# Performance work log

Hardware: AMD Instinct MI355X
Metric: run time of the kernel (lower is better)

## Reference

```python
import jax, jax.numpy as jnp
import numpy as np

B, S, WL = 128, 128, 16
V, C, T = 50000, 100, 17
WE, CE, CF, K, H = 300, 50, 50, 3, 256
D = WE + CF  # LSTM input dim


def setup_inputs() -> dict:
    key = jax.random.key(0)
    ks = jax.random.split(key, 16)
    def n(k, shape, scale=0.05):
        return jax.random.normal(k, shape, jnp.float32) * scale
    words = jax.random.randint(ks[0], (B, S), 0, V)
    chars = jax.random.randint(ks[1], (B, S, WL), 0, C)
    tags = jax.random.randint(ks[2], (B, S), 0, T)
    lengths = jax.random.randint(ks[3], (B,), 1, S + 1)  # at least 1 valid token
    return dict(
        words=words, chars=chars, tags=tags, lengths=lengths,
        word_emb=n(ks[4], (V, WE)).at[0].set(0.0),  # padding_idx=0
        char_emb=n(ks[5], (C, CE)),
        conv_w=n(ks[6], (CF, CE, K)), conv_b=jnp.zeros((CF,), jnp.float32),
        w_ih_f=n(ks[7], (4 * H, D)), w_hh_f=n(ks[8], (4 * H, H)), b_f=jnp.zeros((4 * H,), jnp.float32),
        w_ih_b=n(ks[9], (4 * H, D)), w_hh_b=n(ks[10], (4 * H, H)), b_b=jnp.zeros((4 * H,), jnp.float32),
        proj_w=n(ks[11], (T, 2 * H)), proj_b=jnp.zeros((T,), jnp.float32),
        trans=n(ks[12], (T, T), 0.1), start_trans=n(ks[13], (T,), 0.1), end_trans=n(ks[14], (T,), 0.1),
    )


def _lstm(x, mask, w_ih, w_hh, b):
    # x: [B,S,D], mask: [B,S] bool. PyTorch gate order: i, f, g, o.
    Bh = w_hh.shape[1]
    xg = jnp.einsum('bsd,gd->bsg', x, w_ih) + b  # [B,S,4H]
    def step(carry, inp):
        h, c = carry
        gx, m = inp  # [B,4H], [B]
        g = gx + h @ w_hh.T
        i, f, gg, o = jnp.split(g, 4, axis=-1)
        i = jax.nn.sigmoid(i); f = jax.nn.sigmoid(f)
        gg = jnp.tanh(gg); o = jax.nn.sigmoid(o)
        cn = f * c + i * gg
        hn = o * jnp.tanh(cn)
        m_ = m[:, None]
        return (jnp.where(m_, hn, h), jnp.where(m_, cn, c)), hn * m_
    b_ = x.shape[0]
    init = (jnp.zeros((b_, Bh), x.dtype), jnp.zeros((b_, Bh), x.dtype))
    _, hs = jax.lax.scan(step, init, (jnp.swapaxes(xg, 0, 1), jnp.swapaxes(mask, 0, 1)))
    return jnp.swapaxes(hs, 0, 1)  # [B,S,H]


def _reverse_valid(x, lengths):
    # reverse only the first `length` entries of each row (pack_padded semantics)
    s = x.shape[1]
    t = jnp.arange(s)[None, :]
    idx = jnp.where(t < lengths[:, None], lengths[:, None] - 1 - t, t)
    return jnp.take_along_axis(x, idx[:, :, None], axis=1)


def _crf_nll(emissions, tags, lengths, trans, start_trans, end_trans):
    b, s, t_ = emissions.shape
    mask = jnp.arange(s)[None, :] < lengths[:, None]  # [B,S]
    maskf = mask.astype(emissions.dtype)
    # gold path score
    emit_sc = jnp.take_along_axis(emissions, tags[:, :, None], axis=2)[:, :, 0]  # [B,S]
    score = start_trans[tags[:, 0]] + (emit_sc * maskf).sum(1)
    tr = trans[tags[:, :-1], tags[:, 1:]]  # [B,S-1]
    score = score + (tr * maskf[:, 1:]).sum(1)
    last = jnp.take_along_axis(tags, (lengths - 1)[:, None], axis=1)[:, 0]
    score = score + end_trans[last]
    # partition function (forward algorithm)
    alpha0 = start_trans[None, :] + emissions[:, 0]  # [B,T]
    def step(alpha, inp):
        emit, m = inp  # [B,T], [B]
        nxt = jax.scipy.special.logsumexp(alpha[:, :, None] + trans[None] + emit[:, None, :], axis=1)
        return jnp.where(m[:, None], nxt, alpha), None
    alpha, _ = jax.lax.scan(step, alpha0,
                            (jnp.swapaxes(emissions[:, 1:], 0, 1), jnp.swapaxes(mask[:, 1:], 0, 1)))
    logZ = jax.scipy.special.logsumexp(alpha + end_trans[None, :], axis=-1)
    return jnp.sum(logZ - score)


def reference(words, chars, tags, lengths, word_emb, char_emb, conv_w, conv_b,
              w_ih_f, w_hh_f, b_f, w_ih_b, w_hh_b, b_b, proj_w, proj_b,
              trans, start_trans, end_trans):
    b, s = words.shape
    wl = chars.shape[2]
    we = word_emb[words]  # [B,S,WE]
    ce = char_emb[chars]  # [B,S,WL,CE]
    # CharCNN: conv over word-length, relu, max-pool
    x = ce.reshape(b * s, wl, -1).transpose(0, 2, 1)  # [B*S, CE, WL]
    conv = jax.lax.conv_general_dilated(x, conv_w, (1,), 'SAME',
                                        dimension_numbers=('NCH', 'OIH', 'NCH'))
    conv = conv + conv_b[None, :, None]
    cf = jnp.max(jax.nn.relu(conv), axis=-1).reshape(b, s, -1)  # [B,S,CF]
    inp = jnp.concatenate([we, cf], axis=2)  # [B,S,WE+CF]
    mask = jnp.arange(s)[None, :] < lengths[:, None]
    fwd = _lstm(inp, mask, w_ih_f, w_hh_f, b_f)
    bwd = _reverse_valid(_lstm(_reverse_valid(inp, lengths), mask, w_ih_b, w_hh_b, b_b), lengths)
    h = jnp.concatenate([fwd, bwd], axis=2)  # [B,S,2H]
    emissions = jnp.einsum('bsh,th->bst', h, proj_w) + proj_b
    return _crf_nll(emissions, tags, lengths, trans, start_trans, end_trans)
```

## Files before the change

kernel.cpp:

```cpp
#include <hip/hip_runtime.h>
#include <stdint.h>

typedef unsigned char u8;
typedef unsigned short u16;
typedef unsigned int u32;
typedef unsigned long long u64;

#define NPOS 16384
#define KPAD 384

typedef __attribute__((ext_vector_type(8))) short bf16x8;
typedef __attribute__((ext_vector_type(4))) float f32x4;
typedef __attribute__((ext_vector_type(8))) int i32x8;

__device__ __forceinline__ float bf2f(u16 u) { return __uint_as_float(((u32)u) << 16); }
__device__ __forceinline__ u16 f2bf(float f) {
    u32 u = __float_as_uint(f);
    u += 0x7fffu + ((u >> 16) & 1u);
    return (u16)(u >> 16);
}
__device__ __forceinline__ float frcp(float x) {
#if __has_builtin(__builtin_amdgcn_rcpf)
    return __builtin_amdgcn_rcpf(x);
#else
    return 1.0f / x;
#endif
}
__device__ __forceinline__ float sigm(float x) { return frcp(1.0f + __expf(-x)); }
__device__ __forceinline__ float tanh_(float x) { return fmaf(2.0f, frcp(1.0f + __expf(-2.0f * x)), -1.0f); }

__device__ u8 f2fp8_manual(float f) {
    u32 u = __float_as_uint(f);
    u32 s = (u >> 31) << 7;
    u32 ae = (u >> 23) & 255u;
    u32 m = u & 0x7fffffu;
    int e = (int)ae - 127;
    if (ae == 0) return (u8)s;
    if (e >= 9) return (u8)(s | 0x7e);
    if (e >= -6) {
        u32 mant = m >> 20;
        u32 rem = m & 0xfffffu;
        if (rem > 0x80000u || (rem == 0x80000u && (mant & 1u))) mant++;
        u32 ef = (u32)(e + 7);
        if (mant == 8u) { mant = 0u; ef++; }
        if (ef >= 16u || (ef == 15u && mant == 7u)) return (u8)(s | 0x7e);
        return (u8)(s | (ef << 3) | mant);
    }
    if (e < -10) return (u8)s;
    int sb = 14 - e;
    u32 X = 0x800000u | m;
    u32 mant = X >> sb;
    u32 rem = X & ((1u << sb) - 1u);
    u32 half = 1u << (sb - 1);
    if (rem > half || (rem == half && (mant & 1u))) mant++;
    if (mant >= 8u) return (u8)(s | (1u << 3));
    return (u8)(s | mant);
}

__device__ __forceinline__ u32 f2fp8(float f) {
#if __has_builtin(__builtin_amdgcn_cvt_pk_fp8_f32)
    return (u32)(__builtin_amdgcn_cvt_pk_fp8_f32(f, f, 0, false) & 0xff);
#else
    return (u32)f2fp8_manual(f);
#endif
}

static constexpr size_t OFF_INP  = 0;
static constexpr size_t OFF_WIH  = 12582912;
static constexpr size_t OFF_WHH  = 14155776;
static constexpr size_t OFF_XG   = 15204352;
static constexpr size_t OFF_HS   = 82313216;
static constexpr size_t OFF_EMIS = 99090432;
static constexpr size_t OFF_NLL  = 100204544;
static constexpr size_t OFF_WT   = OFF_XG;

__global__ __launch_bounds__(256) void k_prep0(const float* __restrict__ conv_w,
                                               float* __restrict__ wt) {
    int idx = blockIdx.x * 256 + threadIdx.x;
    if (idx < 7500) {
        int oc = idx / 150, r = idx - oc * 150;
        wt[r * 52 + oc] = conv_w[oc * 150 + r];
    }
}

__global__ __launch_bounds__(256) void k_front(const int* __restrict__ words,
                                               const int* __restrict__ chars,
                                               const float* __restrict__ word_emb,
                                               const float* __restrict__ char_emb,
                                               const float* __restrict__ wt,
                                               const float* __restrict__ conv_b,
                                               u16* __restrict__ inp,
                                               const float* __restrict__ wihf,
                                               const float* __restrict__ wihb,
                                               u16* __restrict__ wih,
                                               const float* __restrict__ whf,
                                               const float* __restrict__ whb,
                                               u8* __restrict__ whh8) {
    __shared__ float ce_t[8][50][20];
    int b = blockIdx.x, tid = threadIdx.x;

    if (b >= 2048) {
        if (b < 3072) {
            int n = (b - 2048) * 2 + (tid >> 7);
            int t128 = tid & 127;
            const float* src = (n < 1024) ? (wihf + (size_t)n * 350) : (wihb + (size_t)(n - 1024) * 350);
            u16* dst = wih + (size_t)n * KPAD;
            for (int k = t128; k < KPAD; k += 128) dst[k] = (k < 350) ? f2bf(src[k]) : (u16)0;
        } else {
            int gr = (b - 3072) * 2 + (tid >> 7);
            int t128 = tid & 127;
            int d = gr >> 10, row = gr & 1023;
            const float* src = (d ? whb : whf) + (size_t)row * 256;
            int g = row >> 8, hid = row & 255;
            int w = hid >> 5, nb = (hid >> 4) & 1, c16 = hid & 15;
            u8* base = whh8 + ((size_t)((d * 8 + w) * 4 + g)) * 8192;
            for (int k = t128; k < 256; k += 128) {
                int kk = k >> 7, q = (k >> 5) & 3, j = k & 31;
                base[((nb * 2 + kk) * 64 + (q * 16 + c16)) * 32 + j] = f2fp8_manual(src[k]);
            }
        }
        return;
    }

    int pos0 = b * 8;

    if (tid < 128) {
        int p = tid >> 4, c = tid & 15;
        int ch = chars[(size_t)(pos0 + p) * 16 + c];
        const float* src = char_emb + (size_t)ch * 50;
#pragma unroll
        for (int i = 0; i < 25; ++i) {
            float2 v = *(const float2*)(src + i * 2);
            ce_t[p][i * 2][c + 1] = v.x;
            ce_t[p][i * 2 + 1][c + 1] = v.y;
        }
    } else {
        int base = tid - 128;
        for (int i = base; i < 1600; i += 128) {
            int p = i / 200, rem = i - p * 200;
            int ic = rem >> 2, cid = rem & 3;
            ce_t[p][ic][cid == 0 ? 0 : 16 + cid] = 0.f;
        }
    }

    for (int r = 0; r < 3; ++r) {
        int idx = r * 256 + tid;
        if (idx < 600) {
            int p = idx / 75, v = idx - p * 75;
            const float4* we4 = (const float4*)(word_emb + (size_t)words[pos0 + p] * 300);
            float4 val = we4[v];
            u64 pk = (u64)f2bf(val.x) | ((u64)f2bf(val.y) << 16) |
                     ((u64)f2bf(val.z) << 32) | ((u64)f2bf(val.w) << 48);
            *(u64*)(inp + (size_t)(pos0 + p) * KPAD + v * 4) = pk;
        }
    }
    {
        int idx = tid;
        if (idx < 136) {
            int p = idx / 17, j = idx - p * 17;
            *(u32*)(inp + (size_t)(pos0 + p) * KPAD + 350 + 2 * j) = 0;
        }
    }
    __syncthreads();

    if (tid < 200) {
        int p = tid / 25, ocp = tid - p * 25;
        int oc = ocp * 2;
        float acc0[16], acc1[16];
#pragma unroll
        for (int t = 0; t < 16; ++t) { acc0[t] = 0.f; acc1[t] = 0.f; }
        const float* cebase = &ce_t[p][0][0];
        for (int ic = 0; ic < 50; ++ic) {
            float c[20];
            const float* cp = cebase + ic * 20;
#pragma unroll
            for (int i = 0; i < 5; ++i) *(float4*)(&c[i * 4]) = *(const float4*)(cp + i * 4);
#pragma unroll
            for (int k = 0; k < 3; ++k) {
                float2 wv = *(const float2*)(wt + (ic * 3 + k) * 52 + oc);
#pragma unroll
                for (int t = 0; t < 16; ++t) {
                    acc0[t] = fmaf(c[t + k], wv.x, acc0[t]);
                    acc1[t] = fmaf(c[t + k], wv.y, acc1[t]);
                }
            }
        }
        float cb0 = conv_b[oc], cb1 = conv_b[oc + 1];
        float m0 = 0.f, m1 = 0.f;
#pragma unroll
        for (int t = 0; t < 16; ++t) {
            m0 = fmaxf(m0, acc0[t] + cb0);
            m1 = fmaxf(m1, acc1[t] + cb1);
        }
        u16* op = inp + (size_t)(pos0 + p) * KPAD + 300 + oc;
        op[0] = f2bf(m0);
        op[1] = f2bf(m1);
    }
}

__global__ __launch_bounds__(256, 2) void k_gemm(const u16* __restrict__ A,
                                                 const u16* __restrict__ Bm,
                                                 u16* __restrict__ C,
                                                 const int* __restrict__ lengths,
                                                 const float* __restrict__ bias_f,
                                                 const float* __restrict__ bias_b) {
    __shared__ u16 sa[128 * 64];
    __shared__ u16 sb[128 * 64];
    int tid = threadIdx.x;
    int dd = blockIdx.x >> 3, hblk = blockIdx.x & 7;
    int m0 = blockIdx.y * 128;
    int lane = tid & 63, wid = tid >> 6;
    int wr = wid >> 1, wc = wid & 1;
    f32x4 acc[4][4];
#pragma unroll
    for (int mt = 0; mt < 4; ++mt)
#pragma unroll
        for (int g = 0; g < 4; ++g) acc[mt][g] = (f32x4){0.f, 0.f, 0.f, 0.f};

    for (int kt = 0; kt < 6; ++kt) {
#pragma unroll
        for (int c = 0; c < 4; ++c) {
            int idx = (c * 256 + tid) * 16;
            int row = idx >> 7, colb = idx & 127;
            int dst = idx ^ ((row & 7) << 4);
            uint4 va = *(const uint4*)((const char*)A + (size_t)(m0 + row) * 768 + kt * 128 + colb);
            *(uint4*)((char*)sa + dst) = va;
            int bmrow = dd * 1024 + (row >> 5) * 256 + hblk * 32 + (row & 31);
            uint4 vb = *(const uint4*)((const char*)Bm + (size_t)bmrow * 768 + kt * 128 + colb);
            *(uint4*)((char*)sb + dst) = vb;
        }
        __syncthreads();
#pragma unroll
        for (int kc = 0; kc < 2; ++kc) {
            bf16x8 af[4], bf[4];
#pragma unroll
            for (int mt = 0; mt < 4; ++mt) {
                int row = wr * 64 + mt * 16 + (lane & 15);
                int off = (row * 128 + kc * 64 + (lane >> 4) * 16) ^ ((row & 7) << 4);
                af[mt] = *(const bf16x8*)((const char*)sa + off);
            }
#pragma unroll
            for (int g = 0; g < 4; ++g) {
                int row = g * 32 + wc * 16 + (lane & 15);
                int off = (row * 128 + kc * 64 + (lane >> 4) * 16) ^ ((row & 7) << 4);
                bf[g] = *(const bf16x8*)((const char*)sb + off);
            }
#pragma unroll
            for (int mt = 0; mt < 4; ++mt)
#pragma unroll
                for (int g = 0; g < 4; ++g)
                    acc[mt][g] = __builtin_amdgcn_mfma_f32_16x16x32_bf16(af[mt], bf[g], acc[mt][g], 0, 0, 0);
        }
        __syncthreads();
    }
    int b = blockIdx.y;
    int len = lengths[b];
    int grp = b >> 4, row16 = b & 15;
    int qq = row16 >> 2, rg = row16 & 3;
    int c16 = lane & 15;
    int hid = hblk * 32 + wc * 16 + c16;
    const float* bias = dd ? bias_b : bias_f;
    float bv[4];
#pragma unroll
    for (int g = 0; g < 4; ++g) bv[g] = bias[g * 256 + hid];
    u32 base16 = (u32)((hblk * 64 + qq * 16 + c16) * 32 + (wc * 4 + rg) * 4);
    size_t slab0 = ((size_t)(dd * 8 + grp) * 128) * 16384;
#pragma unroll
    for (int mt = 0; mt < 4; ++mt)
#pragma unroll
        for (int r = 0; r < 4; ++r) {
            int t = wr * 64 + mt * 16 + (lane >> 4) * 4 + r;
            int tt = dd ? ((t < len) ? (len - 1 - t) : t) : t;
            u64 pk = (u64)f2bf(acc[mt][0][r] + bv[0]) |
                     ((u64)f2bf(acc[mt][1][r] + bv[1]) << 16) |
                     ((u64)f2bf(acc[mt][2][r] + bv[2]) << 32) |
                     ((u64)f2bf(acc[mt][3][r] + bv[3]) << 48);
            *(u64*)(C + slab0 + (size_t)tt * 16384 + base16) = pk;
        }
}

#define LSTM_STEP(T, XC, XN, HA, HW)                                              \
    {                                                                             \
        *(uint4*)(&XN[0])  = *(const uint4*)(xp);                                 \
        *(uint4*)(&XN[4])  = *(const uint4*)(xp + 8);                             \
        *(uint4*)(&XN[8])  = *(const uint4*)(xp + 16);                            \
        *(uint4*)(&XN[12]) = *(const uint4*)(xp + 24);                            \
        xp += 16384;                                                              \
        f32x4 acc[8];                                                             \
        _Pragma("unroll") for (int nb = 0; nb < 2; ++nb)                          \
            _Pragma("unroll") for (int rg = 0; rg < 4; ++rg) {                    \
                int u = nb * 4 + rg;                                              \
                u32 w0 = XC[u * 2], w1 = XC[u * 2 + 1];                           \
                acc[nb * 4 + 0][rg] = __uint_as_float(w0 << 16);                  \
                acc[nb * 4 + 1][rg] = __uint_as_float(w0 & 0xffff0000u);          \
                acc[nb * 4 + 2][rg] = __uint_as_float(w1 << 16);                  \
                acc[nb * 4 + 3][rg] = __uint_as_float(w1 & 0xffff0000u);          \
            }                                                                     \
        i32x8 a0, a1;                                                             \
        *(uint4*)&a0       = *(const uint4*)(HA);                                 \
        *((uint4*)&a0 + 1) = *(const uint4*)(HA + 16);                            \
        *(uint4*)&a1       = *(const uint4*)(HA + 128);                           \
        *((uint4*)&a1 + 1) = *(const uint4*)(HA + 144);                           \
        __builtin_amdgcn_s_setprio(1);                                            \
        _Pragma("unroll") for (int g = 0; g < 4; ++g)                             \
            acc[g] = __builtin_amdgcn_mfma_scale_f32_16x16x128_f8f6f4(            \
                a0, br[g * 4 + 0], acc[g], 0, 0, 0, 127, 0, 127);                 \
        _Pragma("unroll") for (int g = 0; g < 4; ++g)                             \
            acc[g] = __builtin_amdgcn_mfma_scale_f32_16x16x128_f8f6f4(            \
                a1, br[g * 4 + 1], acc[g], 0, 0, 0, 127, 0, 127);                 \
        _Pragma("unroll") for (int g = 0; g < 4; ++g)                             \
            acc[4 + g] = __builtin_amdgcn_mfma_scale_f32_16x16x128_f8f6f4(        \
                a0, br[g * 4 + 2], acc[4 + g], 0, 0, 0, 127, 0, 127);             \
        _Pragma("unroll") for (int g = 0; g < 4; ++g)                             \
            acc[4 + g] = __builtin_amdgcn_mfma_scale_f32_16x16x128_f8f6f4(        \
                a1, br[g * 4 + 3], acc[4 + g], 0, 0, 0, 127, 0, 127);             \
        __builtin_amdgcn_s_setprio(0);                                            \
        _Pragma("unroll") for (int rg = 0; rg < 4; ++rg) {                        \
            bool mv = (T) < lenr[rg];                                             \
            _Pragma("unroll") for (int nb = 0; nb < 2; ++nb) {                    \
                int u = nb * 4 + rg;                                              \
                float gi = sigm(acc[nb * 4 + 0][rg]);                             \
                float gf = sigm(acc[nb * 4 + 1][rg]);                             \
                float gg = tanh_(acc[nb * 4 + 2][rg]);                            \
                float go = sigm(acc[nb * 4 + 3][rg]);                             \
                float cn = gf * cst[u] + gi * gg;                                 \
                float hn = go * tanh_(cn);                                        \
                cst[u] = mv ? cn : cst[u];                                        \
                hbf[u] = mv ? (__float_as_uint(hn) >> 16) : hbf[u];               \
                hq[u]  = mv ? f2fp8(hn) : hq[u];                                  \
                voff[u] += mv ? dstepB : 0;                                       \
                *(u16*)(hsp + voff[u]) = (u16)hbf[u];                             \
                (HW)[rg * 272 + nb * 16] = (u8)hq[u];                             \
            }                                                                     \
        }                                                                         \
        asm volatile("s_waitcnt lgkmcnt(0)\n\ts_barrier" ::: "memory");           \
    }

__global__ __launch_bounds__(512, 2) void k_lstm(const u16* __restrict__ xg2,
                                                 const u8* __restrict__ whh8,
                                                 const int* __restrict__ lengths,
                                                 u16* __restrict__ hs) {
    __shared__ u8 h8[2][4352];
    int tid = threadIdx.x, lane = tid & 63, w = tid >> 6;
    int bx = blockIdx.x;
    int d = bx >> 3, grp = bx & 7;
    int c16 = lane & 15, q = lane >> 4;

    u8* hflat = &h8[0][0];
    for (int i = tid * 8; i < 8704; i += 4096) *(u64*)(hflat + i) = 0;

    int lenr[4];
#pragma unroll
    for (int rg = 0; rg < 4; ++rg) lenr[rg] = lengths[grp * 16 + q * 4 + rg];

    const u8* wbse = whh8 + ((size_t)((d * 8 + w) * 4)) * 8192;
    i32x8 br[16];
#pragma unroll
    for (int g = 0; g < 4; ++g)
#pragma unroll
        for (int nb = 0; nb < 2; ++nb)
#pragma unroll
            for (int kk = 0; kk < 2; ++kk) {
                const u8* p = wbse + (size_t)g * 8192 + ((nb * 2 + kk) * 64 + lane) * 32;
                i32x8 v;
                *(uint4*)&v       = *(const uint4*)p;
                *((uint4*)&v + 1) = *(const uint4*)(p + 16);
                br[g * 4 + nb * 2 + kk] = v;
            }

    float cst[8];
    u32 hq[8], hbf[8];
#pragma unroll
    for (int u = 0; u < 8; ++u) { cst[u] = 0.f; hq[u] = 0; hbf[u] = 0; }

    u32 voff[8];
    int dstepB = d ? -1024 : 1024;
    u8* hsp = (u8*)hs;
#pragma unroll
    for (int nb = 0; nb < 2; ++nb)
#pragma unroll
        for (int rg = 0; rg < 4; ++rg) {
            int u = nb * 4 + rg;
            int row = q * 4 + rg;
            int hid = w * 32 + nb * 16 + c16;
            int p0 = d ? (lenr[rg] - 1) : 0;
            voff[u] = (u32)((((grp * 16 + row) * 128 + p0) * 512 + d * 256 + hid) * 2 - dstepB);
        }

    const u16* xslab = xg2 + ((size_t)(d * 8 + grp) * 128) * 16384 + (w * 64 + lane) * 32;
    u32 xqa[16], xqb[16];
    *(uint4*)(&xqa[0])  = *(const uint4*)(xslab);
    *(uint4*)(&xqa[4])  = *(const uint4*)(xslab + 8);
    *(uint4*)(&xqa[8])  = *(const uint4*)(xslab + 16);
    *(uint4*)(&xqa[12]) = *(const uint4*)(xslab + 24);
    const u16* xp = xslab + 16384;

    const u8* ha0 = hflat + (c16 * 272 + q * 32);
    const u8* ha1 = ha0 + 4352;
    u8* hw1 = hflat + (q * 1088 + w * 32 + c16);
    u8* hw0 = hw1 + 4352;

    __syncthreads();

    for (int t2 = 0; t2 < 128; t2 += 2) {
        LSTM_STEP(t2,     xqa, xqb, ha0, hw0)
        LSTM_STEP(t2 + 1, xqb, xqa, ha1, hw1)
    }
}

__global__ __launch_bounds__(256) void k_emis(const u16* __restrict__ hs,
                                              const float* __restrict__ proj_w,
                                              const float* __restrict__ proj_b,
                                              float* __restrict__ emis) {
    __shared__ float pw[17 * 512];
    int tid = threadIdx.x;
    for (int i = tid; i < 17 * 512; i += 256) pw[i] = proj_w[i];
    __syncthreads();
    int lane = tid & 63, wv = tid >> 6;
    int pos0 = blockIdx.x * 16 + wv * 4;
    float hv[4][8];
#pragma unroll
    for (int p = 0; p < 4; ++p) {
        bf16x8 v = *(const bf16x8*)(hs + (size_t)(pos0 + p) * 512 + lane * 8);
#pragma unroll
        for (int j = 0; j < 8; ++j) hv[p][j] = bf2f((u16)v[j]);
    }
    for (int tg = 0; tg < 17; ++tg) {
        const float* wp = pw + tg * 512 + lane * 8;
        float wr[8];
#pragma unroll
        for (int j = 0; j < 8; ++j) wr[j] = wp[j];
        float s[4];
#pragma unroll
        for (int p = 0; p < 4; ++p) {
            float acc = 0.f;
#pragma unroll
            for (int j = 0; j < 8; ++j) acc = fmaf(hv[p][j], wr[j], acc);
            s[p] = acc;
        }
#pragma unroll
        for (int off = 32; off; off >>= 1)
#pragma unroll
            for (int p = 0; p < 4; ++p) s[p] += __shfl_down(s[p], off);
        if (lane == 0) {
#pragma unroll
            for (int p = 0; p < 4; ++p) emis[(size_t)(pos0 + p) * 17 + tg] = s[p] + proj_b[tg];
        }
    }
}

__global__ __launch_bounds__(64) void k_crf(const float* __restrict__ emis,
                                            const int* __restrict__ tags,
                                            const int* __restrict__ lengths,
                                            const float* __restrict__ trans,
                                            const float* __restrict__ start_trans,
                                            const float* __restrict__ end_trans,
                                            float* __restrict__ nll) {
    int b = blockIdx.x, lane = threadIdx.x;
    __shared__ float tr[289];
    __shared__ float al[17];
    __shared__ float scs;
    for (int i = lane; i < 289; i += 64) tr[i] = trans[i];
    int len = lengths[b];
    const int* tg = tags + (size_t)b * 128;
    const float* em = emis + (size_t)b * 128 * 17;
    __syncthreads();

    float sc = 0.f;
    for (int t = lane; t < len; t += 64) {
        sc += em[t * 17 + tg[t]];
        if (t >= 1) sc += tr[tg[t - 1] * 17 + tg[t]];
    }
#pragma unroll
    for (int off = 32; off; off >>= 1) sc += __shfl_down(sc, off);
    if (lane == 0) scs = sc + start_trans[tg[0]] + end_trans[tg[len - 1]];

    if (lane < 17) al[lane] = start_trans[lane] + em[lane];
    __syncthreads();
    for (int t = 1; t < len; ++t) {
        float anew = 0.f;
        if (lane < 17) {
            float m = -1e30f;
            for (int i = 0; i < 17; ++i) m = fmaxf(m, al[i] + tr[i * 17 + lane]);
            float s = 0.f;
            for (int i = 0; i < 17; ++i) s += __expf(al[i] + tr[i * 17 + lane] - m);
            anew = m + __logf(s) + em[t * 17 + lane];
        }
        __syncthreads();
        if (lane < 17) al[lane] = anew;
        __syncthreads();
    }
    float v = (lane < 17) ? al[lane] + end_trans[lane] : -1e30f;
    float m = v;
#pragma unroll
    for (int off = 32; off; off >>= 1) m = fmaxf(m, __shfl_xor(m, off));
    float s = (lane < 17) ? __expf(v - m) : 0.f;
#pragma unroll
    for (int off = 32; off; off >>= 1) s += __shfl_xor(s, off);
    if (lane == 0) nll[b] = (m + __logf(s)) - scs;
}

__global__ __launch_bounds__(128) void k_reduce(const float* __restrict__ nll, float* __restrict__ out) {
    int tid = threadIdx.x;
    float v = nll[tid];
#pragma unroll
    for (int off = 32; off; off >>= 1) v += __shfl_down(v, off);
    __shared__ float partial[2];
    if ((tid & 63) == 0) partial[tid >> 6] = v;
    __syncthreads();
    if (tid == 0) out[0] = partial[0] + partial[1];
}

extern "C" void kernel_launch(void* const* d_in, const int* in_sizes, int n_in,
                              void* d_out, int out_size, void* d_ws, size_t ws_size,
                              hipStream_t stream) {
    (void)in_sizes; (void)n_in; (void)out_size; (void)ws_size;
    const int*   words       = (const int*)d_in[0];
    const int*   chars       = (const int*)d_in[1];
    const int*   tags        = (const int*)d_in[2];
    const int*   lengths     = (const int*)d_in[3];
    const float* word_emb    = (const float*)d_in[4];
    const float* char_emb    = (const float*)d_in[5];
    const float* conv_w      = (const float*)d_in[6];
    const float* conv_b      = (const float*)d_in[7];
    const float* w_ih_f      = (const float*)d_in[8];
    const float* w_hh_f      = (const float*)d_in[9];
    const float* b_f         = (const float*)d_in[10];
    const float* w_ih_b      = (const float*)d_in[11];
    const float* w_hh_b      = (const float*)d_in[12];
    const float* b_b         = (const float*)d_in[13];
    const float* proj_w      = (const float*)d_in[14];
    const float* proj_b      = (const float*)d_in[15];
    const float* trans       = (const float*)d_in[16];
    const float* start_trans = (const float*)d_in[17];
    const float* end_trans   = (const float*)d_in[18];

    char* ws = (char*)d_ws;
    u16* inp   = (u16*)(ws + OFF_INP);
    u16* wih   = (u16*)(ws + OFF_WIH);
    u8*  whh8  = (u8*)(ws + OFF_WHH);
    u16* xgb   = (u16*)(ws + OFF_XG);
    u16* hsb   = (u16*)(ws + OFF_HS);
    float* em  = (float*)(ws + OFF_EMIS);
    float* nll = (float*)(ws + OFF_NLL);
    float* wt  = (float*)(ws + OFF_WT);

    k_prep0<<<30, 256, 0, stream>>>(conv_w, wt);
    k_front<<<4096, 256, 0, stream>>>(words, chars, word_emb, char_emb, wt, conv_b, inp,
                                      w_ih_f, w_ih_b, wih, w_hh_f, w_hh_b, whh8);
    k_gemm<<<dim3(16, 128), 256, 0, stream>>>(inp, wih, xgb, lengths, b_f, b_b);
    k_lstm<<<16, 512, 0, stream>>>(xgb, whh8, lengths, hsb);
    k_emis<<<1024, 256, 0, stream>>>(hsb, proj_w, proj_b, em);
    k_crf<<<128, 64, 0, stream>>>(em, tags, lengths, trans, start_trans, end_trans, nll);
    k_reduce<<<1, 128, 0, stream>>>(nll, (float*)d_out);
}
```

Measured before the change: 445.9 us.

## Skip padded positions across front, GEMM, LSTM and emission kernels

Uses per-sequence lengths to skip work on padded timesteps. The front kernel exits early for blocks lying entirely past the length. The GEMM skips MFMA and stores for row tiles beyond the length. The LSTM stops its time loop at the group's maximum length, and the emission kernel skips blocks past the length. This removes roughly half of the work, since lengths are uniform in 1..128. The risk is that downstream readers such as the CRF, or the masked LSTM reads, touch uninitialized padded entries, so correctness depends on those values always being masked.

```diff
diff --git a/kernel.cpp b/kernel.cpp
--- a/kernel.cpp
+++ b/kernel.cpp
@@ -95,7 +95,8 @@
                                                u16* __restrict__ wih,
                                                const float* __restrict__ whf,
                                                const float* __restrict__ whb,
-                                               u8* __restrict__ whh8) {
+                                               u8* __restrict__ whh8,
+                                               const int* __restrict__ lengths) {
     __shared__ float ce_t[8][50][20];
     int b = blockIdx.x, tid = threadIdx.x;
 
@@ -122,6 +123,8 @@
         return;
     }
 
+    if (((b & 15) * 8) >= lengths[b >> 4]) return;
+
     int pos0 = b * 8;
 
     if (tid < 128) {
@@ -211,6 +214,11 @@
     int m0 = blockIdx.y * 128;
     int lane = tid & 63, wid = tid >> 6;
     int wr = wid >> 1, wc = wid & 1;
+    int b = blockIdx.y;
+    int len = lengths[b];
+    int lenS = __builtin_amdgcn_readfirstlane(len);
+    int wrS = __builtin_amdgcn_readfirstlane(wr);
+
     f32x4 acc[4][4];
 #pragma unroll
     for (int mt = 0; mt < 4; ++mt)
@@ -232,13 +240,7 @@
         __syncthreads();
 #pragma unroll
         for (int kc = 0; kc < 2; ++kc) {
-            bf16x8 af[4], bf[4];
-#pragma unroll
-            for (int mt = 0; mt < 4; ++mt) {
-                int row = wr * 64 + mt * 16 + (lane & 15);
-                int off = (row * 128 + kc * 64 + (lane >> 4) * 16) ^ ((row & 7) << 4);
-                af[mt] = *(const bf16x8*)((const char*)sa + off);
-            }
+            bf16x8 bf[4];
 #pragma unroll
             for (int g = 0; g < 4; ++g) {
                 int row = g * 32 + wc * 16 + (lane & 15);
@@ -246,15 +248,19 @@
                 bf[g] = *(const bf16x8*)((const char*)sb + off);
             }
 #pragma unroll
-            for (int mt = 0; mt < 4; ++mt)
-#pragma unroll
-                for (int g = 0; g < 4; ++g)
-                    acc[mt][g] = __builtin_amdgcn_mfma_f32_16x16x32_bf16(af[mt], bf[g], acc[mt][g], 0, 0, 0);
+            for (int mt = 0; mt < 4; ++mt) {
+                if (wrS * 64 + mt * 16 < lenS) {
+                    int row = wr * 64 + mt * 16 + (lane & 15);
+                    int off = (row * 128 + kc * 64 + (lane >> 4) * 16) ^ ((row & 7) << 4);
+                    bf16x8 af = *(const bf16x8*)((const char*)sa + off);
+#pragma unroll
+                    for (int g = 0; g < 4; ++g)
+                        acc[mt][g] = __builtin_amdgcn_mfma_f32_16x16x32_bf16(af, bf[g], acc[mt][g], 0, 0, 0);
+                }
+            }
         }
         __syncthreads();
     }
-    int b = blockIdx.y;
-    int len = lengths[b];
     int grp = b >> 4, row16 = b & 15;
     int qq = row16 >> 2, rg = row16 & 3;
     int c16 = lane & 15;
@@ -266,17 +272,20 @@
     u32 base16 = (u32)((hblk * 64 + qq * 16 + c16) * 32 + (wc * 4 + rg) * 4);
     size_t slab0 = ((size_t)(dd * 8 + grp) * 128) * 16384;
 #pragma unroll
-    for (int mt = 0; mt < 4; ++mt)
-#pragma unroll
-        for (int r = 0; r < 4; ++r) {
-            int t = wr * 64 + mt * 16 + (lane >> 4) * 4 + r;
-            int tt = dd ? ((t < len) ? (len - 1 - t) : t) : t;
-            u64 pk = (u64)f2bf(acc[mt][0][r] + bv[0]) |
-                     ((u64)f2bf(acc[mt][1][r] + bv[1]) << 16) |
-                     ((u64)f2bf(acc[mt][2][r] + bv[2]) << 32) |
-                     ((u64)f2bf(acc[mt][3][r] + bv[3]) << 48);
-            *(u64*)(C + slab0 + (size_t)tt * 16384 + base16) = pk;
-        }
+    for (int mt = 0; mt < 4; ++mt) {
+        if (wrS * 64 + mt * 16 < lenS) {
+#pragma unroll
+            for (int r = 0; r < 4; ++r) {
+                int t = wr * 64 + mt * 16 + (lane >> 4) * 4 + r;
+                int tt = dd ? ((t < len) ? (len - 1 - t) : t) : t;
+                u64 pk = (u64)f2bf(acc[mt][0][r] + bv[0]) |
+                         ((u64)f2bf(acc[mt][1][r] + bv[1]) << 16) |
+                         ((u64)f2bf(acc[mt][2][r] + bv[2]) << 32) |
+                         ((u64)f2bf(acc[mt][3][r] + bv[3]) << 48);
+                *(u64*)(C + slab0 + (size_t)tt * 16384 + base16) = pk;
+            }
+        }
+    }
 }
 
 #define LSTM_STEP(T, XC, XN, HA, HW)                                              \
@@ -353,6 +362,15 @@
 #pragma unroll
     for (int rg = 0; rg < 4; ++rg) lenr[rg] = lengths[grp * 16 + q * 4 + rg];
 
+    int ml = lenr[0];
+#pragma unroll
+    for (int rg = 1; rg < 4; ++rg) ml = ml > lenr[rg] ? ml : lenr[rg];
+    {
+        int o = __shfl_xor(ml, 16); ml = ml > o ? ml : o;
+        o = __shfl_xor(ml, 32);     ml = ml > o ? ml : o;
+    }
+    int tmax = (ml + 1) & ~1;
+
     const u8* wbse = whh8 + ((size_t)((d * 8 + w) * 4)) * 8192;
     i32x8 br[16];
 #pragma unroll
@@ -402,7 +420,7 @@
 
     __syncthreads();
 
-    for (int t2 = 0; t2 < 128; t2 += 2) {
+    for (int t2 = 0; t2 < tmax; t2 += 2) {
         LSTM_STEP(t2,     xqa, xqb, ha0, hw0)
         LSTM_STEP(t2 + 1, xqb, xqa, ha1, hw1)
     }
@@ -411,13 +429,17 @@
 __global__ __launch_bounds__(256) void k_emis(const u16* __restrict__ hs,
                                               const float* __restrict__ proj_w,
                                               const float* __restrict__ proj_b,
-                                              float* __restrict__ emis) {
+                                              float* __restrict__ emis,
+                                              const int* __restrict__ lengths) {
+    int p00 = blockIdx.x * 16;
+    if ((p00 & 127) >= lengths[p00 >> 7]) return;
+
     __shared__ float pw[17 * 512];
     int tid = threadIdx.x;
     for (int i = tid; i < 17 * 512; i += 256) pw[i] = proj_w[i];
     __syncthreads();
     int lane = tid & 63, wv = tid >> 6;
-    int pos0 = blockIdx.x * 16 + wv * 4;
+    int pos0 = p00 + wv * 4;
     float hv[4][8];
 #pragma unroll
     for (int p = 0; p < 4; ++p) {
@@ -547,10 +569,10 @@
 
     k_prep0<<<30, 256, 0, stream>>>(conv_w, wt);
     k_front<<<4096, 256, 0, stream>>>(words, chars, word_emb, char_emb, wt, conv_b, inp,
-                                      w_ih_f, w_ih_b, wih, w_hh_f, w_hh_b, whh8);
+                                      w_ih_f, w_ih_b, wih, w_hh_f, w_hh_b, whh8, lengths);
     k_gemm<<<dim3(16, 128), 256, 0, stream>>>(inp, wih, xgb, lengths, b_f, b_b);
     k_lstm<<<16, 512, 0, stream>>>(xgb, whh8, lengths, hsb);
-    k_emis<<<1024, 256, 0, stream>>>(hsb, proj_w, proj_b, em);
+    k_emis<<<1024, 256, 0, stream>>>(hsb, proj_w, proj_b, em, lengths);
     k_crf<<<128, 64, 0, stream>>>(em, tags, lengths, trans, start_trans, end_trans, nll);
     k_reduce<<<1, 128, 0, stream>>>(nll, (float*)d_out);
 }
```

Result: faster. 435.4 us (-2.3%).
